# Optimization experiments

Measured on AMD Instinct MI355X. Metric: run time of the kernel, lower is better.

## Reference

```python
import jax, jax.numpy as jnp
import numpy as np

NODE_DIM = 64
HIDDEN_DIM = 128
N_GRAPHS = 8
NODES_PER_GRAPH = 2048
N_TOTAL = N_GRAPHS * NODES_PER_GRAPH
N_EDGES = N_TOTAL * 32


def setup_inputs() -> dict:
    key = jax.random.key(0)
    ks = jax.random.split(key, 8)
    x = jax.random.normal(ks[0], (N_TOTAL, NODE_DIM), dtype=jnp.float32)
    edge_index = jax.random.randint(ks[1], (2, N_EDGES), 0, N_TOTAL, dtype=jnp.int64)
    # NNConv root weights + biases (glorot-ish scale)
    W1 = jax.random.normal(ks[2], (NODE_DIM, HIDDEN_DIM), dtype=jnp.float32) / np.sqrt(NODE_DIM)
    b1 = jnp.zeros((HIDDEN_DIM,), dtype=jnp.float32)
    W2 = jax.random.normal(ks[3], (HIDDEN_DIM, HIDDEN_DIM), dtype=jnp.float32) / np.sqrt(HIDDEN_DIM)
    b2 = jnp.zeros((HIDDEN_DIM,), dtype=jnp.float32)
    # link-predictor Linear(2*hidden -> 1)
    w_lin = jax.random.normal(ks[4], (2 * HIDDEN_DIM,), dtype=jnp.float32) / np.sqrt(2 * HIDDEN_DIM)
    b_lin = jnp.zeros((), dtype=jnp.float32)
    return {
        "x": x, "edge_index": edge_index,
        "W1": W1, "b1": b1, "W2": W2, "b2": b2,
        "w_lin": w_lin, "b_lin": b_lin,
        "n_graphs": N_GRAPHS, "nodes_per_graph": NODES_PER_GRAPH,
    }


def _nnconv_ones(x, src, dst, W_root, bias, n_total):
    # callable_my returns ones(in*out) -> per-edge weight matrix is all-ones [in,out],
    # so message_e = x[src_e] @ ones = sum(x[src_e]) broadcast over out channels.
    s = x.sum(axis=-1)                         # [N]
    msg = jnp.take(s, src, axis=0)             # [E]
    agg = jax.ops.segment_sum(msg, dst, num_segments=n_total)           # [N]
    deg = jax.ops.segment_sum(jnp.ones_like(msg), dst, num_segments=n_total)
    agg = agg / jnp.where(deg > 0, deg, 1.0)   # mean aggregation; 0 for isolated nodes
    return agg[:, None] + x @ W_root + bias    # [N, out]


def reference(x, edge_index, W1, b1, W2, b2, w_lin, b_lin, n_graphs, nodes_per_graph):
    n_total = n_graphs * nodes_per_graph
    src, dst = edge_index[0], edge_index[1]
    # dropout layers are identity in eval mode
    h = jax.nn.relu(_nnconv_ones(x, src, dst, W1, b1, n_total))
    h = jax.nn.relu(_nnconv_ones(h, src, dst, W2, b2, n_total))
    # all-pairs concat + Linear(2H->1) + sigmoid, per graph, vectorized:
    # score[b,i,j] = sigmoid(h[b,i].w_left + h[b,j].w_right + b)
    H = h.shape[-1]
    hb = h.reshape(n_graphs, nodes_per_graph, H)
    left = hb @ w_lin[:H]                      # [B, N]
    right = hb @ w_lin[H:]                     # [B, N]
    scores = jax.nn.sigmoid(left[:, :, None] + right[:, None, :] + b_lin)
    # original returns a tuple of per-graph flat [N*N] tensors; equal sizes -> [B, N*N]
    return scores.reshape(n_graphs, nodes_per_graph * nodes_per_graph)
```

## Files before the change

kernel.cpp:

```cpp
#include <hip/hip_runtime.h>

#define N_TOTAL 16384
#define NODE_DIM 64
#define HIDDEN 128
#define NPG 2048
#define NGRAPH 8
#define NPART 64

typedef float v4f __attribute__((ext_vector_type(4)));

#define C1      (1 << 19)
#define SC1     8192.0f
#define ISC1    (1.0f / 8192.0f)
#define SC2     16384.0f
#define ISC2    (1.0f / 16384.0f)

__device__ __forceinline__ int detect_flag(const int* ei_words) {
    int lane = threadIdx.x & 63;
    int nz = 0;
    for (int i = lane; i < 256; i += 64)
        if (ei_words[2 * i + 1] != 0) nz = 1;
    return __any(nz) ? 1 : 0;
}

__global__ __launch_bounds__(256) void kS1(
    const float* __restrict__ x, float* __restrict__ s1) {
    int tid = threadIdx.x;
    int r   = blockIdx.x * 16 + (tid >> 4);
    int q   = tid & 15;
    float4 v = ((const float4*)x)[r * 16 + q];
    float sum = v.x + v.y + v.z + v.w;
    sum += __shfl_xor(sum, 1);
    sum += __shfl_xor(sum, 2);
    sum += __shfl_xor(sum, 4);
    sum += __shfl_xor(sum, 8);
    if (q == 0) s1[r] = sum;
}

__global__ __launch_bounds__(512) void kScat1(
    const void* __restrict__ ei_raw, int E, const float* __restrict__ s1,
    unsigned* __restrict__ pcomb, unsigned* __restrict__ dec) {
    __shared__ unsigned acc[N_TOTAL];
    int tid = threadIdx.x, b = blockIdx.x;
    int f = detect_flag((const int*)ei_raw);
    for (int i = tid; i < N_TOTAL; i += 512) acc[i] = 0u;
    __syncthreads();
    int epb = (E + NPART - 1) / NPART;
    int e0 = b * epb, e1 = min(E, e0 + epb);
    if (f) {
        const int* ep = (const int*)ei_raw;
        for (int e = e0 + tid; e < e1; e += 512) {
            int src = ep[e], dst = ep[E + e];
            dec[e] = (unsigned)src | ((unsigned)dst << 16);
            int q = (int)lrintf(s1[src] * SC1);
            atomicAdd(&acc[dst], (1u << 26) + (unsigned)(q + C1));
        }
    } else {
        const long long* ep = (const long long*)ei_raw;
        for (int e = e0 + tid; e < e1; e += 512) {
            int src = (int)ep[e], dst = (int)ep[E + e];
            dec[e] = (unsigned)src | ((unsigned)dst << 16);
            int q = (int)lrintf(s1[src] * SC1);
            atomicAdd(&acc[dst], (1u << 26) + (unsigned)(q + C1));
        }
    }
    __syncthreads();
    unsigned* outp = pcomb + (size_t)b * N_TOTAL;
    for (int i = tid; i < N_TOTAL; i += 512) outp[i] = acc[i];
}

__global__ __launch_bounds__(512) void kScat2(
    const unsigned* __restrict__ dec, int E, const float* __restrict__ s2,
    int* __restrict__ ps2) {
    __shared__ int acc[N_TOTAL];
    int tid = threadIdx.x, b = blockIdx.x;
    for (int i = tid; i < N_TOTAL; i += 512) acc[i] = 0;
    __syncthreads();
    int epb = (E + NPART - 1) / NPART;
    int e0 = b * epb, e1 = min(E, e0 + epb);
    for (int e = e0 + tid; e < e1; e += 512) {
        unsigned d32 = dec[e];
        int src = (int)(d32 & 0xFFFFu), dst = (int)(d32 >> 16);
        int q = (int)lrintf(s2[src] * SC2);
        atomicAdd((unsigned*)&acc[dst], (unsigned)q);
    }
    __syncthreads();
    int* outp = ps2 + (size_t)b * N_TOTAL;
    for (int i = tid; i < N_TOTAL; i += 512) outp[i] = acc[i];
}

__global__ __launch_bounds__(256) void k3_layer1(
    const float* __restrict__ x, const float* __restrict__ W1,
    const float* __restrict__ b1, const unsigned* __restrict__ pcomb,
    float* __restrict__ h1, float* __restrict__ s2, float* __restrict__ degf) {
    __shared__ float W1s[NODE_DIM * HIDDEN];
    __shared__ float xs[32 * NODE_DIM];
    __shared__ float mean1s[32];
    int tid  = threadIdx.x;
    int base = blockIdx.x * 32;
    {
        int r = tid >> 3, j = tid & 7;
        int grow = base + r;
        int c = 0, sq = 0;
        #pragma unroll
        for (int k = 0; k < 8; ++k) {
            unsigned v = pcomb[(size_t)(j + 8 * k) * N_TOTAL + grow];
            int n_i = (int)(v >> 26);
            c  += n_i;
            sq += (int)(v & 0x03FFFFFFu) - n_i * C1;
        }
        for (int off = 4; off; off >>= 1) {
            c  += __shfl_xor(c, off);
            sq += __shfl_xor(sq, off);
        }
        if (j == 0) {
            mean1s[r] = c > 0 ? ((float)sq * ISC1) / (float)c : 0.f;
            degf[grow] = (float)c;
        }
    }
    {
        const float4* Wv = (const float4*)W1;
        float4* Wsv = (float4*)W1s;
        for (int i = tid; i < NODE_DIM * HIDDEN / 4; i += 256) Wsv[i] = Wv[i];
        const float4* xv = (const float4*)(x + base * NODE_DIM);
        float4* xsv = (float4*)xs;
        for (int i = tid; i < 32 * NODE_DIM / 4; i += 256) xsv[i] = xv[i];
    }
    __syncthreads();
    int lane32 = tid & 31;
    int rg     = tid >> 5;
    int c4     = lane32 * 4;
    int r0     = rg * 4;
    float a[4][4];
    #pragma unroll
    for (int i = 0; i < 4; ++i)
        #pragma unroll
        for (int jj = 0; jj < 4; ++jj) a[i][jj] = 0.f;
    #pragma unroll
    for (int k = 0; k < NODE_DIM; ++k) {
        float4 w = *(const float4*)&W1s[k * HIDDEN + c4];
        #pragma unroll
        for (int i = 0; i < 4; ++i) {
            float xv = xs[(r0 + i) * NODE_DIM + k];
            a[i][0] = fmaf(xv, w.x, a[i][0]);
            a[i][1] = fmaf(xv, w.y, a[i][1]);
            a[i][2] = fmaf(xv, w.z, a[i][2]);
            a[i][3] = fmaf(xv, w.w, a[i][3]);
        }
    }
    float4 bb = *(const float4*)&b1[c4];
    #pragma unroll
    for (int i = 0; i < 4; ++i) {
        int row  = r0 + i;
        int grow = base + row;
        float mean = mean1s[row];
        v4f v;
        v.x = fmaxf(mean + a[i][0] + bb.x, 0.f);
        v.y = fmaxf(mean + a[i][1] + bb.y, 0.f);
        v.z = fmaxf(mean + a[i][2] + bb.z, 0.f);
        v.w = fmaxf(mean + a[i][3] + bb.w, 0.f);
        __builtin_nontemporal_store(v, (v4f*)&h1[grow * HIDDEN + c4]);
        float rs = v.x + v.y + v.z + v.w;
        for (int off = 16; off; off >>= 1) rs += __shfl_xor(rs, off);
        if (lane32 == 0) s2[grow] = rs;
    }
}

__global__ __launch_bounds__(256) void k6_layer2(
    const float* __restrict__ h1, const float* __restrict__ W2,
    const float* __restrict__ b2, const int* __restrict__ ps2,
    const float* __restrict__ degf, const float* __restrict__ wlin,
    float* __restrict__ left, float* __restrict__ right) {
    __shared__ float W2s[64 * HIDDEN];
    __shared__ float hs[32 * HIDDEN];
    __shared__ float mean2s[32];
    int tid  = threadIdx.x;
    int base = blockIdx.x * 32;
    {
        int r = tid >> 3, j = tid & 7;
        int grow = base + r;
        int sq = 0;
        #pragma unroll
        for (int k = 0; k < 8; ++k)
            sq += ps2[(size_t)(j + 8 * k) * N_TOTAL + grow];
        for (int off = 4; off; off >>= 1) sq += __shfl_xor(sq, off);
        if (j == 0) {
            float d = degf[grow];
            mean2s[r] = d > 0.f ? ((float)sq * ISC2) / d : 0.f;
        }
    }
    {
        const float4* hv = (const float4*)(h1 + base * HIDDEN);
        float4* hsv = (float4*)hs;
        for (int i = tid; i < 32 * HIDDEN / 4; i += 256) hsv[i] = hv[i];
    }
    int lane32 = tid & 31;
    int rg     = tid >> 5;
    int c4     = lane32 * 4;
    int r0     = rg * 4;
    float a[4][4];
    #pragma unroll
    for (int i = 0; i < 4; ++i)
        #pragma unroll
        for (int jj = 0; jj < 4; ++jj) a[i][jj] = 0.f;
    for (int chunk = 0; chunk < 2; ++chunk) {
        __syncthreads();
        {
            const float4* Wv = (const float4*)(W2 + chunk * 64 * HIDDEN);
            float4* Wsv = (float4*)W2s;
            for (int i = tid; i < 64 * HIDDEN / 4; i += 256) Wsv[i] = Wv[i];
        }
        __syncthreads();
        int kb = chunk * 64;
        #pragma unroll 8
        for (int k = 0; k < 64; ++k) {
            float4 w = *(const float4*)&W2s[k * HIDDEN + c4];
            #pragma unroll
            for (int i = 0; i < 4; ++i) {
                float hv = hs[(r0 + i) * HIDDEN + kb + k];
                a[i][0] = fmaf(hv, w.x, a[i][0]);
                a[i][1] = fmaf(hv, w.y, a[i][1]);
                a[i][2] = fmaf(hv, w.z, a[i][2]);
                a[i][3] = fmaf(hv, w.w, a[i][3]);
            }
        }
    }
    float4 bb  = *(const float4*)&b2[c4];
    float4 wl  = *(const float4*)&wlin[c4];
    float4 wr  = *(const float4*)&wlin[HIDDEN + c4];
    #pragma unroll
    for (int i = 0; i < 4; ++i) {
        int row  = r0 + i;
        int grow = base + row;
        float ag = mean2s[row];
        float h0e = fmaxf(ag + a[i][0] + bb.x, 0.f);
        float h1e = fmaxf(ag + a[i][1] + bb.y, 0.f);
        float h2e = fmaxf(ag + a[i][2] + bb.z, 0.f);
        float h3e = fmaxf(ag + a[i][3] + bb.w, 0.f);
        float lp = h0e * wl.x + h1e * wl.y + h2e * wl.z + h3e * wl.w;
        float rp = h0e * wr.x + h1e * wr.y + h2e * wr.z + h3e * wr.w;
        for (int off = 16; off; off >>= 1) {
            lp += __shfl_xor(lp, off);
            rp += __shfl_xor(rp, off);
        }
        if (lane32 == 0) { left[grow] = lp; right[grow] = rp; }
    }
}

__global__ __launch_bounds__(256) void k7_scores(
    const float* __restrict__ left, const float* __restrict__ right,
    const float* __restrict__ blin, float* __restrict__ out) {
    int tid  = threadIdx.x;
    int base = blockIdx.x * 16;
    float bl = blin[0];
    const v4f* rv4 = (const v4f*)(right + ((base >> 11) << 11));
    #pragma unroll 4
    for (int rr = 0; rr < 16; ++rr) {
        int r = base + rr;
        float L = left[r] + bl;
        v4f* orow = (v4f*)out + ((size_t)r << 9);
        #pragma unroll
        for (int c = tid; c < 512; c += 256) {
            v4f rv = rv4[c];
            v4f o;
            o.x = 1.f / (1.f + __expf(-(L + rv.x)));
            o.y = 1.f / (1.f + __expf(-(L + rv.y)));
            o.z = 1.f / (1.f + __expf(-(L + rv.z)));
            o.w = 1.f / (1.f + __expf(-(L + rv.w)));
            __builtin_nontemporal_store(o, orow + c);
        }
    }
}

extern "C" void kernel_launch(void* const* d_in, const int* in_sizes, int n_in,
                              void* d_out, int out_size, void* d_ws, size_t ws_size,
                              hipStream_t stream) {
    const float* x    = (const float*)d_in[0];
    const void*  ei   = d_in[1];
    const float* W1   = (const float*)d_in[2];
    const float* b1   = (const float*)d_in[3];
    const float* W2   = (const float*)d_in[4];
    const float* b2   = (const float*)d_in[5];
    const float* wlin = (const float*)d_in[6];
    const float* blin = (const float*)d_in[7];
    int E = in_sizes[1] / 2;

    float* ws    = (float*)d_ws;
    float* s1    = ws;
    float* s2    = ws + 1 * N_TOTAL;
    float* degf  = ws + 2 * N_TOTAL;
    float* left  = ws + 3 * N_TOTAL;
    float* right = ws + 4 * N_TOTAL;
    float* h1    = ws + 5 * N_TOTAL;
    unsigned* dec = (unsigned*)(h1 + (size_t)HIDDEN * N_TOTAL);
    float* out   = (float*)d_out;

    unsigned* pcomb = (unsigned*)d_out;
    int*      ps2   = (int*)d_out + (size_t)NPART * N_TOTAL;

    kS1<<<N_TOTAL / 16, 256, 0, stream>>>(x, s1);
    kScat1<<<NPART, 512, 0, stream>>>(ei, E, s1, pcomb, dec);
    k3_layer1<<<N_TOTAL / 32, 256, 0, stream>>>(x, W1, b1, pcomb, h1, s2, degf);
    kScat2<<<NPART, 512, 0, stream>>>(dec, E, s2, ps2);
    k6_layer2<<<N_TOTAL / 32, 256, 0, stream>>>(h1, W2, b2, ps2, degf, wlin, left, right);
    k7_scores<<<N_TOTAL / 16, 256, 0, stream>>>(left, right, blin, out);
}
```

Measured before the change: 90.19 us.

## Fuse row-sum into scatter, double partitions, vectorize edge loads

Removes the separate kS1 row-sum kernel and instead recomputes each source node's 64-float row sum inside kScat1 for every edge. The number of scatter partitions doubles to 128 blocks, and edge indices and decoded words are now processed four at a time with vector loads. The partial-reduction readers in layer1 and layer2 are restructured to sum 128 partials with a coalesced layout and a shared-memory reduction. The trade-off is one less kernel launch against 32x redundant gathers of x rows (256 bytes per edge instead of 4), plus twice as many partial buffers to zero, write and read.

```diff
diff --git a/kernel.cpp b/kernel.cpp
--- a/kernel.cpp
+++ b/kernel.cpp
@@ -5,7 +5,7 @@
 #define HIDDEN 128
 #define NPG 2048
 #define NGRAPH 8
-#define NPART 64
+#define NPART 128
 
 typedef float v4f __attribute__((ext_vector_type(4)));
 
@@ -23,45 +23,87 @@
     return __any(nz) ? 1 : 0;
 }
 
-__global__ __launch_bounds__(256) void kS1(
-    const float* __restrict__ x, float* __restrict__ s1) {
-    int tid = threadIdx.x;
-    int r   = blockIdx.x * 16 + (tid >> 4);
-    int q   = tid & 15;
-    float4 v = ((const float4*)x)[r * 16 + q];
-    float sum = v.x + v.y + v.z + v.w;
-    sum += __shfl_xor(sum, 1);
-    sum += __shfl_xor(sum, 2);
-    sum += __shfl_xor(sum, 4);
-    sum += __shfl_xor(sum, 8);
-    if (q == 0) s1[r] = sum;
+__device__ __forceinline__ float rowsum_x(const float* __restrict__ x, int row) {
+    const float4* xr = (const float4*)(x + row * NODE_DIM);
+    float4 a = xr[0];
+    #pragma unroll
+    for (int j = 1; j < 16; ++j) a += xr[j];
+    return a.x + a.y + a.z + a.w;
 }
 
 __global__ __launch_bounds__(512) void kScat1(
-    const void* __restrict__ ei_raw, int E, const float* __restrict__ s1,
+    const void* __restrict__ ei_raw, int E, const float* __restrict__ x,
     unsigned* __restrict__ pcomb, unsigned* __restrict__ dec) {
     __shared__ unsigned acc[N_TOTAL];
     int tid = threadIdx.x, b = blockIdx.x;
     int f = detect_flag((const int*)ei_raw);
     for (int i = tid; i < N_TOTAL; i += 512) acc[i] = 0u;
     __syncthreads();
-    int epb = (E + NPART - 1) / NPART;
+    int epb = (((E + NPART - 1) / NPART) + 3) & ~3;
     int e0 = b * epb, e1 = min(E, e0 + epb);
-    if (f) {
-        const int* ep = (const int*)ei_raw;
-        for (int e = e0 + tid; e < e1; e += 512) {
-            int src = ep[e], dst = ep[E + e];
-            dec[e] = (unsigned)src | ((unsigned)dst << 16);
-            int q = (int)lrintf(s1[src] * SC1);
-            atomicAdd(&acc[dst], (1u << 26) + (unsigned)(q + C1));
-        }
-    } else {
-        const long long* ep = (const long long*)ei_raw;
-        for (int e = e0 + tid; e < e1; e += 512) {
-            int src = (int)ep[e], dst = (int)ep[E + e];
-            dec[e] = (unsigned)src | ((unsigned)dst << 16);
-            int q = (int)lrintf(s1[src] * SC1);
-            atomicAdd(&acc[dst], (1u << 26) + (unsigned)(q + C1));
+    int count = e1 - e0;
+    if (count > 0) {
+        int groups = count >> 2;
+        if (f) {
+            const int* ep  = (const int*)ei_raw;
+            const int* epd = ep + E;
+            for (int g = tid; g < groups; g += 512) {
+                int eb = e0 + g * 4;
+                int4 s4 = *(const int4*)(ep + eb);
+                int4 d4 = *(const int4*)(epd + eb);
+                float v0 = rowsum_x(x, s4.x), v1 = rowsum_x(x, s4.y);
+                float v2 = rowsum_x(x, s4.z), v3 = rowsum_x(x, s4.w);
+                uint4 dw;
+                dw.x = (unsigned)s4.x | ((unsigned)d4.x << 16);
+                dw.y = (unsigned)s4.y | ((unsigned)d4.y << 16);
+                dw.z = (unsigned)s4.z | ((unsigned)d4.z << 16);
+                dw.w = (unsigned)s4.w | ((unsigned)d4.w << 16);
+                *(uint4*)(dec + eb) = dw;
+                atomicAdd(&acc[d4.x], (1u << 26) + (unsigned)((int)lrintf(v0 * SC1) + C1));
+                atomicAdd(&acc[d4.y], (1u << 26) + (unsigned)((int)lrintf(v1 * SC1) + C1));
+                atomicAdd(&acc[d4.z], (1u << 26) + (unsigned)((int)lrintf(v2 * SC1) + C1));
+                atomicAdd(&acc[d4.w], (1u << 26) + (unsigned)((int)lrintf(v3 * SC1) + C1));
+            }
+            int rem0 = e0 + groups * 4;
+            if (tid < e1 - rem0) {
+                int e = rem0 + tid;
+                int s = ep[e], d = epd[e];
+                dec[e] = (unsigned)s | ((unsigned)d << 16);
+                float v = rowsum_x(x, s);
+                atomicAdd(&acc[d], (1u << 26) + (unsigned)((int)lrintf(v * SC1) + C1));
+            }
+        } else {
+            const long long* ep  = (const long long*)ei_raw;
+            const long long* epd = ep + E;
+            for (int g = tid; g < groups; g += 512) {
+                int eb = e0 + g * 4;
+                longlong2 sa = *(const longlong2*)(ep + eb);
+                longlong2 sb = *(const longlong2*)(ep + eb + 2);
+                longlong2 da = *(const longlong2*)(epd + eb);
+                longlong2 db = *(const longlong2*)(epd + eb + 2);
+                int s0 = (int)sa.x, s1i = (int)sa.y, s2i = (int)sb.x, s3 = (int)sb.y;
+                int d0 = (int)da.x, d1 = (int)da.y, d2 = (int)db.x, d3 = (int)db.y;
+                float v0 = rowsum_x(x, s0), v1 = rowsum_x(x, s1i);
+                float v2 = rowsum_x(x, s2i), v3 = rowsum_x(x, s3);
+                uint4 dw;
+                dw.x = (unsigned)s0  | ((unsigned)d0 << 16);
+                dw.y = (unsigned)s1i | ((unsigned)d1 << 16);
+                dw.z = (unsigned)s2i | ((unsigned)d2 << 16);
+                dw.w = (unsigned)s3  | ((unsigned)d3 << 16);
+                *(uint4*)(dec + eb) = dw;
+                atomicAdd(&acc[d0], (1u << 26) + (unsigned)((int)lrintf(v0 * SC1) + C1));
+                atomicAdd(&acc[d1], (1u << 26) + (unsigned)((int)lrintf(v1 * SC1) + C1));
+                atomicAdd(&acc[d2], (1u << 26) + (unsigned)((int)lrintf(v2 * SC1) + C1));
+                atomicAdd(&acc[d3], (1u << 26) + (unsigned)((int)lrintf(v3 * SC1) + C1));
+            }
+            int rem0 = e0 + groups * 4;
+            if (tid < e1 - rem0) {
+                int e = rem0 + tid;
+                int s = (int)ep[e], d = (int)epd[e];
+                dec[e] = (unsigned)s | ((unsigned)d << 16);
+                float v = rowsum_x(x, s);
+                atomicAdd(&acc[d], (1u << 26) + (unsigned)((int)lrintf(v * SC1) + C1));
+            }
         }
     }
     __syncthreads();
@@ -76,13 +118,27 @@
     int tid = threadIdx.x, b = blockIdx.x;
     for (int i = tid; i < N_TOTAL; i += 512) acc[i] = 0;
     __syncthreads();
-    int epb = (E + NPART - 1) / NPART;
+    int epb = (((E + NPART - 1) / NPART) + 3) & ~3;
     int e0 = b * epb, e1 = min(E, e0 + epb);
-    for (int e = e0 + tid; e < e1; e += 512) {
-        unsigned d32 = dec[e];
-        int src = (int)(d32 & 0xFFFFu), dst = (int)(d32 >> 16);
-        int q = (int)lrintf(s2[src] * SC2);
-        atomicAdd((unsigned*)&acc[dst], (unsigned)q);
+    int count = e1 - e0;
+    if (count > 0) {
+        int groups = count >> 2;
+        for (int g = tid; g < groups; g += 512) {
+            int eb = e0 + g * 4;
+            uint4 dw = *(const uint4*)(dec + eb);
+            float v0 = s2[dw.x & 0xFFFFu], v1 = s2[dw.y & 0xFFFFu];
+            float v2 = s2[dw.z & 0xFFFFu], v3 = s2[dw.w & 0xFFFFu];
+            atomicAdd((unsigned*)&acc[dw.x >> 16], (unsigned)(int)lrintf(v0 * SC2));
+            atomicAdd((unsigned*)&acc[dw.y >> 16], (unsigned)(int)lrintf(v1 * SC2));
+            atomicAdd((unsigned*)&acc[dw.z >> 16], (unsigned)(int)lrintf(v2 * SC2));
+            atomicAdd((unsigned*)&acc[dw.w >> 16], (unsigned)(int)lrintf(v3 * SC2));
+        }
+        int rem0 = e0 + groups * 4;
+        if (tid < e1 - rem0) {
+            unsigned d32 = dec[rem0 + tid];
+            float v = s2[d32 & 0xFFFFu];
+            atomicAdd((unsigned*)&acc[d32 >> 16], (unsigned)(int)lrintf(v * SC2));
+        }
     }
     __syncthreads();
     int* outp = ps2 + (size_t)b * N_TOTAL;
@@ -96,27 +152,23 @@
     __shared__ float W1s[NODE_DIM * HIDDEN];
     __shared__ float xs[32 * NODE_DIM];
     __shared__ float mean1s[32];
+    __shared__ int redc[4][32], reds[4][32];
     int tid  = threadIdx.x;
     int base = blockIdx.x * 32;
     {
-        int r = tid >> 3, j = tid & 7;
-        int grow = base + r;
+        int r = tid & 31, jg = tid >> 5;
         int c = 0, sq = 0;
         #pragma unroll
-        for (int k = 0; k < 8; ++k) {
-            unsigned v = pcomb[(size_t)(j + 8 * k) * N_TOTAL + grow];
+        for (int k = 0; k < 16; ++k) {
+            unsigned v = pcomb[(size_t)(jg * 16 + k) * N_TOTAL + base + r];
             int n_i = (int)(v >> 26);
             c  += n_i;
             sq += (int)(v & 0x03FFFFFFu) - n_i * C1;
         }
-        for (int off = 4; off; off >>= 1) {
-            c  += __shfl_xor(c, off);
-            sq += __shfl_xor(sq, off);
-        }
-        if (j == 0) {
-            mean1s[r] = c > 0 ? ((float)sq * ISC1) / (float)c : 0.f;
-            degf[grow] = (float)c;
-        }
+        c  += __shfl_xor(c, 32);
+        sq += __shfl_xor(sq, 32);
+        int w = tid >> 6, l = tid & 63;
+        if (l < 32) { redc[w][l] = c; reds[w][l] = sq; }
     }
     {
         const float4* Wv = (const float4*)W1;
@@ -125,6 +177,13 @@
         const float4* xv = (const float4*)(x + base * NODE_DIM);
         float4* xsv = (float4*)xs;
         for (int i = tid; i < 32 * NODE_DIM / 4; i += 256) xsv[i] = xv[i];
+    }
+    __syncthreads();
+    if (tid < 32) {
+        int C = redc[0][tid] + redc[1][tid] + redc[2][tid] + redc[3][tid];
+        int S = reds[0][tid] + reds[1][tid] + reds[2][tid] + reds[3][tid];
+        mean1s[tid] = C > 0 ? ((float)S * ISC1) / (float)C : 0.f;
+        degf[base + tid] = (float)C;
     }
     __syncthreads();
     int lane32 = tid & 31;
@@ -174,25 +233,29 @@
     __shared__ float W2s[64 * HIDDEN];
     __shared__ float hs[32 * HIDDEN];
     __shared__ float mean2s[32];
+    __shared__ int reds[4][32];
     int tid  = threadIdx.x;
     int base = blockIdx.x * 32;
     {
-        int r = tid >> 3, j = tid & 7;
-        int grow = base + r;
+        int r = tid & 31, jg = tid >> 5;
         int sq = 0;
         #pragma unroll
-        for (int k = 0; k < 8; ++k)
-            sq += ps2[(size_t)(j + 8 * k) * N_TOTAL + grow];
-        for (int off = 4; off; off >>= 1) sq += __shfl_xor(sq, off);
-        if (j == 0) {
-            float d = degf[grow];
-            mean2s[r] = d > 0.f ? ((float)sq * ISC2) / d : 0.f;
-        }
+        for (int k = 0; k < 16; ++k)
+            sq += ps2[(size_t)(jg * 16 + k) * N_TOTAL + base + r];
+        sq += __shfl_xor(sq, 32);
+        int w = tid >> 6, l = tid & 63;
+        if (l < 32) reds[w][l] = sq;
     }
     {
         const float4* hv = (const float4*)(h1 + base * HIDDEN);
         float4* hsv = (float4*)hs;
         for (int i = tid; i < 32 * HIDDEN / 4; i += 256) hsv[i] = hv[i];
+    }
+    __syncthreads();
+    if (tid < 32) {
+        int S = reds[0][tid] + reds[1][tid] + reds[2][tid] + reds[3][tid];
+        float d = degf[base + tid];
+        mean2s[tid] = d > 0.f ? ((float)S * ISC2) / d : 0.f;
     }
     int lane32 = tid & 31;
     int rg     = tid >> 5;
@@ -286,20 +349,18 @@
     int E = in_sizes[1] / 2;
 
     float* ws    = (float*)d_ws;
-    float* s1    = ws;
-    float* s2    = ws + 1 * N_TOTAL;
-    float* degf  = ws + 2 * N_TOTAL;
-    float* left  = ws + 3 * N_TOTAL;
-    float* right = ws + 4 * N_TOTAL;
-    float* h1    = ws + 5 * N_TOTAL;
+    float* s2    = ws;
+    float* degf  = ws + 1 * N_TOTAL;
+    float* left  = ws + 2 * N_TOTAL;
+    float* right = ws + 3 * N_TOTAL;
+    float* h1    = ws + 4 * N_TOTAL;
     unsigned* dec = (unsigned*)(h1 + (size_t)HIDDEN * N_TOTAL);
     float* out   = (float*)d_out;
 
     unsigned* pcomb = (unsigned*)d_out;
     int*      ps2   = (int*)d_out + (size_t)NPART * N_TOTAL;
 
-    kS1<<<N_TOTAL / 16, 256, 0, stream>>>(x, s1);
-    kScat1<<<NPART, 512, 0, stream>>>(ei, E, s1, pcomb, dec);
+    kScat1<<<NPART, 512, 0, stream>>>(ei, E, x, pcomb, dec);
     k3_layer1<<<N_TOTAL / 32, 256, 0, stream>>>(x, W1, b1, pcomb, h1, s2, degf);
     kScat2<<<NPART, 512, 0, stream>>>(dec, E, s2, ps2);
     k6_layer2<<<N_TOTAL / 32, 256, 0, stream>>>(h1, W2, b2, ps2, degf, wlin, left, right);
```

Result: slower. 117.2 us (+30.0%).
